# Performance work log

Hardware: AMD Instinct MI355X
Metric: run time of the kernel (lower is better)

The kernel has to match this reference:

```python
import jax, jax.numpy as jnp
import numpy as np

B, L, F, H, VOCAB = 32, 700, 4, 600, 2000  # batch, n_records(max_len), feats/record, hidden, vocab


def setup_inputs() -> dict:
    key = jax.random.key(0)
    ks = jax.random.split(key, 16)
    s = 0.02
    inp = {
        'records': jax.random.randint(ks[0], (B, L, F), 0, VOCAB, dtype=jnp.int64 if jax.config.jax_enable_x64 else jnp.int32),
        'index': jax.random.randint(ks[1], (B,), 0, L, dtype=jnp.int32),
        'emb': jax.random.normal(ks[2], (VOCAB, H), jnp.float32) * s,
        'W_relu': jax.random.normal(ks[3], (4 * H, H), jnp.float32) * s,
        'b_relu': jnp.zeros((H,), jnp.float32),
        'W_lin': jax.random.normal(ks[4], (H, H), jnp.float32) * s,
        'b_lin': jnp.zeros((H,), jnp.float32),
        'W_sig': jax.random.normal(ks[5], (2 * H, H), jnp.float32) * s,
        'b_sig': jnp.zeros((H,), jnp.float32),
        'W_ih': jax.random.normal(ks[6], (H, 4 * H), jnp.float32) * s,
        'W_hh': jax.random.normal(ks[7], (H, 4 * H), jnp.float32) * s,
        'b_ih': jnp.zeros((4 * H,), jnp.float32),
        'b_hh': jnp.zeros((4 * H,), jnp.float32),
        'W_log': jax.random.normal(ks[8], (H, L), jnp.float32) * s,
        'b_log': jnp.zeros((L,), jnp.float32),
    }
    return inp


def _select_content(records, emb, W_relu, b_relu, W_lin, b_lin, W_sig, b_sig):
    # embedding + concat of the 4 record features -> [B, L, 4H]
    embedded = emb[records]                               # [B, L, 4, H]
    emb_cat = embedded.reshape(records.shape[0], records.shape[1], -1)
    emb_relu = jax.nn.relu(emb_cat @ W_relu + b_relu)      # [B, L, H]
    emb_lin = emb_relu @ W_lin + b_lin                     # [B, L, H]
    pre_attn = jnp.einsum('bld,bmd->blm', emb_lin, emb_relu)  # [B, L, L]
    pad = (records.max(axis=2) == 0)                       # [B, L]
    mask = jnp.eye(records.shape[1], dtype=bool)[None] | pad[:, :, None] | pad[:, None, :]
    pre_attn = jnp.where(mask, -jnp.inf, pre_attn)
    attention = jax.nn.softmax(pre_attn, axis=2)
    emb_att = jnp.einsum('blm,bmd->bld', attention, emb_relu)  # [B, L, H]
    gate = jax.nn.sigmoid(jnp.concatenate([emb_relu, emb_att], axis=2) @ W_sig + b_sig)
    return gate * emb_relu                                 # selected_content [B, L, H]


def reference(records, index, emb, W_relu, b_relu, W_lin, b_lin, W_sig, b_sig,
              W_ih, W_hh, b_ih, b_hh, W_log, b_log):
    sc = _select_content(records, emb, W_relu, b_relu, W_lin, b_lin, W_sig, b_sig)
    # init_hidden
    hidden = jnp.mean(sc, axis=1)                          # [B, H]
    cell = jnp.zeros_like(hidden)
    pad_mask = (records.max(axis=2) == 0)                  # [B, L]
    # forward (one pointer step)
    b_idx = jnp.arange(records.shape[0])
    mask = pad_mask.at[b_idx, index].set(True)             # scatter_(1, index, 1)
    x = sc[b_idx, index]                                   # gather -> [B, H]
    gates = x @ W_ih + hidden @ W_hh + b_ih + b_hh         # [B, 4H]
    i, f, g, o = jnp.split(gates, 4, axis=1)               # torch LSTM gate order
    cell = jax.nn.sigmoid(f) * cell + jax.nn.sigmoid(i) * jnp.tanh(g)
    hidden = jax.nn.sigmoid(o) * jnp.tanh(cell)
    logits = hidden @ W_log + b_log                        # [B, max_len]
    masked = jnp.where(mask, -jnp.inf, logits)
    attention = jax.nn.log_softmax(masked, axis=1)         # [B, max_len]
    return attention, hidden, cell
```

## Files before the change

kernel.cpp:

```cpp
#include <hip/hip_runtime.h>
#include <math.h>

typedef unsigned short u16;
typedef _Float16 half8 __attribute__((ext_vector_type(8)));
typedef float f32x4 __attribute__((ext_vector_type(4)));

#define BB 32
#define LL 700
#define HH 600
#define VV 2000
#define H4 2400

#define O_SCAT   0L
#define O_LINH   57344000L
#define O_R1     86016000L
#define O_ATTNH  112896000L
#define O_ERT    144435200L
#define O_EMBH   171468800L
#define O_W2T    174028800L
#define O_WLT    177100800L
#define O_WST    177920000L
#define O_BL     179456000L
#define O_PAD    179458560L
#define O_GATES  179624960L
#define O_WIHT   179932160L
#define O_WLOGT  186076160L
#define O_XCAT   186977280L
#define O_HID16  187059200L
#define O_GLOG   187100160L
#define O_XMEAN  187190272L

__device__ inline u16 f2h(float x) { _Float16 h = (_Float16)x; u16 u; __builtin_memcpy(&u, &h, 2); return u; }
__device__ inline float h2f(u16 u) { _Float16 h; __builtin_memcpy(&h, &u, 2); return (float)h; }
__device__ inline float to_f(float x) { return x; }
__device__ inline float to_f(u16 x) { return h2f(x); }

__device__ __forceinline__ void gll16(const u16* g, u16* l) {
    __builtin_amdgcn_global_load_lds(
        (__attribute__((address_space(1))) void*)g,
        (__attribute__((address_space(3))) void*)l, 16, 0, 0);
}

template<int EPI>
__global__ __launch_bounds__(512, 4) void hgemm_v2(
    const u16* __restrict__ A, const u16* __restrict__ B,
    u16* __restrict__ C16, const float* __restrict__ bias,
    const u16* __restrict__ gate, int ldg,
    float* __restrict__ xmean,
    int M, int N, int Kp, int lda, int ldb, int ldc,
    long sAz, long sBz, long sCz)
{
    const int bz = blockIdx.z;
    A += sAz * bz;  B += sBz * bz;  C16 += sCz * bz;

    __shared__ __align__(16) u16 As[16384];
    __shared__ __align__(16) u16 Bs[16384];

    const int tid = threadIdx.x;

    const int nx = gridDim.x, ny = gridDim.y;
    const int bid = blockIdx.y * nx + blockIdx.x;
    const int fg  = ny >> 3;
    const int gsz = nx << 3;
    int m_i, n_i;
    if (bid < fg * gsz) {
        int g = bid / gsz, r = bid - g * gsz;
        m_i = (g << 3) + (r & 7);
        n_i = r >> 3;
    } else {
        m_i = bid / nx;
        n_i = bid - m_i * nx;
    }
    const int m0 = m_i << 7, n0 = n_i << 7;

    const int wave = tid >> 6, lane = tid & 63;
    const int fr = lane & 15, q = lane >> 4;
    const int s0 = (q ^ (fr & 7)) << 3;
    const int wm = (wave >> 2) << 6;
    const int wn = (wave & 3) << 5;

    const int srow = lane >> 3;
    const int kx   = ((lane & 7) ^ srow) << 3;
    int ra0 = m0 + (wave << 4) + srow;       if (ra0 > M - 1) ra0 = M - 1;
    int ra1 = m0 + (wave << 4) + 8 + srow;   if (ra1 > M - 1) ra1 = M - 1;
    int rb0 = n0 + (wave << 4) + srow;       if (rb0 > N - 1) rb0 = N - 1;
    int rb1 = n0 + (wave << 4) + 8 + srow;   if (rb1 > N - 1) rb1 = N - 1;
    const u16* gA0 = A + (long)ra0 * lda + kx;
    const u16* gA1 = A + (long)ra1 * lda + kx;
    const u16* gB0 = B + (long)rb0 * ldb + kx;
    const u16* gB1 = B + (long)rb1 * ldb + kx;
    u16* sAw = (u16*)As + (wave << 10);
    u16* sBw = (u16*)Bs + (wave << 10);

    f32x4 acc[4][2];
    #pragma unroll
    for (int i = 0; i < 4; ++i)
        #pragma unroll
        for (int j = 0; j < 2; ++j) acc[i][j] = (f32x4)0.f;

    const int nk = Kp >> 6;

    gll16(gA0, sAw);  gll16(gA1, sAw + 512);
    gll16(gB0, sBw);  gll16(gB1, sBw + 512);
    __syncthreads();

    for (int t = 0; t < nk; ++t) {
        const int cur = (t & 1) << 13;
        if (t + 1 < nk) {
            const int nxt = cur ^ 8192;
            const long ko = (long)(t + 1) << 6;
            gll16(gA0 + ko, sAw + nxt);  gll16(gA1 + ko, sAw + nxt + 512);
            gll16(gB0 + ko, sBw + nxt);  gll16(gB1 + ko, sBw + nxt + 512);
        }
        #pragma unroll
        for (int half = 0; half < 2; ++half) {
            const int sh = s0 ^ (half << 5);
            half8 af[4], bf[2];
            #pragma unroll
            for (int i = 0; i < 4; ++i)
                af[i] = *(const half8*)&As[cur + ((wm + (i << 4) + fr) << 6) + sh];
            #pragma unroll
            for (int j = 0; j < 2; ++j)
                bf[j] = *(const half8*)&Bs[cur + ((wn + (j << 4) + fr) << 6) + sh];
            #pragma unroll
            for (int i = 0; i < 4; ++i)
                #pragma unroll
                for (int j = 0; j < 2; ++j)
                    acc[i][j] = __builtin_amdgcn_mfma_f32_16x16x32_f16(af[i], bf[j], acc[i][j], 0, 0, 0);
        }
        __syncthreads();
    }

    const int lr = (lane >> 4) << 2;
    #pragma unroll
    for (int j = 0; j < 2; ++j) {
        int n = n0 + wn + (j << 4) + fr;
        if (n >= N) continue;
        float bv = bias ? bias[n] : 0.f;
        float ps = 0.f;
        int   cb = -1;
        #pragma unroll
        for (int i = 0; i < 4; ++i) {
            #pragma unroll
            for (int r = 0; r < 4; ++r) {
                int m = m0 + wm + (i << 4) + lr + r;
                if (m >= M) continue;
                long off = (long)m * ldc + n;
                float v = acc[i][j][r] + bv;
                if (EPI == 1) C16[off] = f2h(v);
                if (EPI == 2) {
                    float sg = 1.f / (1.f + expf(-v));
                    float scv = sg * h2f(gate[(long)m * ldg + n]);
                    C16[off] = f2h(scv);
                    int b = m / 700;
                    if (b != cb) {
                        if (cb >= 0) atomicAdd(&xmean[cb * 640 + n], ps);
                        cb = b;  ps = 0.f;
                    }
                    ps += scv;
                }
            }
        }
        if (EPI == 2 && cb >= 0) atomicAdd(&xmean[cb * 640 + n], ps);
    }
}

__global__ __launch_bounds__(256) void sgemm_k(
    const u16* __restrict__ A, const u16* __restrict__ B, float* __restrict__ C,
    int N, int Kseg, int lda, int ldb, int ldc)
{
    const int wave = threadIdx.x >> 6, lane = threadIdx.x & 63;
    const int fr = lane & 15, q8 = (lane >> 4) << 3;
    int n = blockIdx.x * 64 + wave * 16 + fr;
    int nc = (n < N) ? n : N - 1;
    const int k0 = blockIdx.y * Kseg;
    const u16* pa0 = A + (long)fr * lda + q8;
    const u16* pa1 = A + (long)(fr + 16) * lda + q8;
    const u16* pb  = B + (long)nc * ldb + q8;
    f32x4 acc0 = (f32x4)0.f, acc1 = (f32x4)0.f;
    #pragma unroll 2
    for (int k = k0; k < k0 + Kseg; k += 32) {
        half8 a0 = *(const half8*)(pa0 + k);
        half8 a1 = *(const half8*)(pa1 + k);
        half8 bv = *(const half8*)(pb + k);
        acc0 = __builtin_amdgcn_mfma_f32_16x16x32_f16(a0, bv, acc0, 0, 0, 0);
        acc1 = __builtin_amdgcn_mfma_f32_16x16x32_f16(a1, bv, acc1, 0, 0, 0);
    }
    if (n >= N) return;
    const int mr = (lane >> 4) << 2;
    #pragma unroll
    for (int r = 0; r < 4; ++r) {
        atomicAdd(&C[(long)(mr + r) * ldc + n], acc0[r]);
        atomicAdd(&C[(long)(mr + r + 16) * ldc + n], acc1[r]);
    }
}

__global__ __launch_bounds__(256) void prep_k(
    const float* __restrict__ emb, const float* __restrict__ W_relu,
    const float* __restrict__ W_lin, const float* __restrict__ W_sig,
    const float* __restrict__ W_ih, const float* __restrict__ W_hh,
    const float* __restrict__ W_log, const float* __restrict__ b_lin,
    const float* __restrict__ b_ih, const float* __restrict__ b_hh,
    const float* __restrict__ b_log,
    u16* __restrict__ embh, u16* __restrict__ w2t, u16* __restrict__ wlt,
    u16* __restrict__ wst, u16* __restrict__ wiht, u16* __restrict__ wlogt,
    float* __restrict__ bl640, float* __restrict__ gates, float* __restrict__ glog,
    float* __restrict__ xmean)
{
    __shared__ float t[32][33];
    const int z = blockIdx.z, bx = blockIdx.x, by = blockIdx.y;
    const int tid = threadIdx.x;

    if (z == 10) {
        int r = by * 32 + (tid >> 5), c = bx * 32 + (tid & 31);
        #pragma unroll
        for (int dy = 0; dy < 32; dy += 8) {
            int rr = r + dy;
            if (rr < VV && c < 640)
                embh[(long)rr * 640 + c] = (c < 600) ? f2h(emb[(long)rr * 600 + c]) : 0;
        }
        return;
    }
    if (z == 11) {
        long idx = ((long)bx * 75 + by) * 256 + tid;
        const long NG = 640 + (long)BB * H4;
        const long NL = NG + (long)BB * 704;
        const long NX = NL + (long)BB * 640;
        if (idx < 640) {
            bl640[idx] = (idx < 600) ? b_lin[idx] : 0.f;
        } else if (idx < NG) {
            long i = idx - 640;
            int n = (int)(i % H4);
            gates[i] = b_ih[n] + b_hh[n];
        } else if (idx < NL) {
            long i = idx - NG;
            int l = (int)(i % 704);
            glog[i] = (l < 700) ? b_log[l] : 0.f;
        } else if (idx < NX) {
            xmean[idx - NL] = 0.f;
        }
        return;
    }

    const float* s; u16* d;
    int R, C, lds_, ldo, Rpad, Cpad;
    if (z < 4)      { s = W_relu + 360000L * z; d = w2t + 384000L * z;
                      R = 600; C = 600; lds_ = 600; ldo = 640;  Rpad = 640; Cpad = 600; }
    else if (z == 4){ s = W_lin;           d = wlt;
                      R = 600; C = 600; lds_ = 600; ldo = 640;  Rpad = 640; Cpad = 640; }
    else if (z == 5){ s = W_sig;           d = wst;
                      R = 600; C = 600; lds_ = 600; ldo = 1280; Rpad = 640; Cpad = 600; }
    else if (z == 6){ s = W_sig + 360000;  d = wst + 640;
                      R = 600; C = 600; lds_ = 600; ldo = 1280; Rpad = 640; Cpad = 600; }
    else if (z == 7){ s = W_ih;            d = wiht;
                      R = 600; C = H4;  lds_ = H4;  ldo = 1280; Rpad = 640; Cpad = H4; }
    else if (z == 8){ s = W_hh;            d = wiht + 640;
                      R = 600; C = H4;  lds_ = H4;  ldo = 1280; Rpad = 640; Cpad = H4; }
    else            { s = W_log;           d = wlogt;
                      R = 600; C = 700; lds_ = 700; ldo = 640;  Rpad = 640; Cpad = 704; }

    int r0 = bx * 32, c0 = by * 32;
    if (r0 >= Rpad || c0 >= Cpad) return;
    int tx = tid & 31, ty = tid >> 5;
    #pragma unroll
    for (int dy = 0; dy < 32; dy += 8) {
        int r = r0 + ty + dy, c = c0 + tx;
        t[ty + dy][tx] = (r < R && c < C) ? s[(long)r * lds_ + c] : 0.f;
    }
    __syncthreads();
    #pragma unroll
    for (int dy = 0; dy < 32; dy += 8) {
        int c = c0 + ty + dy, r = r0 + tx;
        if (r < Rpad && c < Cpad) d[(long)c * ldo + r] = f2h(t[tx][ty + dy]);
    }
}

template<typename T>
__global__ __launch_bounds__(256) void transpz_k(
    const T* __restrict__ s, u16* __restrict__ d,
    int R, int C, int lds_, int ldo, int Rpad, int Cpad, long zs_s, long zs_d)
{
    __shared__ float t[32][33];
    s += zs_s * blockIdx.z;  d += zs_d * blockIdx.z;
    int r0 = blockIdx.x * 32, c0 = blockIdx.y * 32;
    int tx = threadIdx.x & 31, ty = threadIdx.x >> 5;
    #pragma unroll
    for (int dy = 0; dy < 32; dy += 8) {
        int r = r0 + ty + dy, c = c0 + tx;
        t[ty + dy][tx] = (r < R && c < C) ? to_f(s[(long)r * lds_ + c]) : 0.f;
    }
    __syncthreads();
    #pragma unroll
    for (int dy = 0; dy < 32; dy += 8) {
        int c = c0 + ty + dy, r = r0 + tx;
        if (r < Rpad && c < Cpad) d[(long)c * ldo + r] = f2h(t[tx][ty + dy]);
    }
}

__global__ __launch_bounds__(320) void gather_relu_k(
    const int* __restrict__ rec, const u16* __restrict__ Ph,
    const float* __restrict__ b_relu, u16* __restrict__ scat, float* __restrict__ pad)
{
    int row = blockIdx.x;
    int t = threadIdx.x;
    int r0 = rec[row * 4 + 0], r1 = rec[row * 4 + 1];
    int r2 = rec[row * 4 + 2], r3 = rec[row * 4 + 3];
    u16* srow = scat + (long)row * 1280;
    if (t < 300) {
        int h = t << 1;
        uint a0 = *(const uint*)&Ph[(long)r0 * H4 + h];
        uint a1 = *(const uint*)&Ph[(long)r1 * H4 + 600 + h];
        uint a2 = *(const uint*)&Ph[(long)r2 * H4 + 1200 + h];
        uint a3 = *(const uint*)&Ph[(long)r3 * H4 + 1800 + h];
        float lo = b_relu[h]     + h2f((u16)a0) + h2f((u16)a1) + h2f((u16)a2) + h2f((u16)a3);
        float hi = b_relu[h + 1] + h2f((u16)(a0 >> 16)) + h2f((u16)(a1 >> 16))
                                 + h2f((u16)(a2 >> 16)) + h2f((u16)(a3 >> 16));
        uint o = (uint)f2h(fmaxf(lo, 0.f)) | ((uint)f2h(fmaxf(hi, 0.f)) << 16);
        *(uint*)&srow[h] = o;
    } else {
        int i = t - 300;
        *(uint*)&srow[600 + (i << 1)]  = 0;
        *(uint*)&srow[1240 + (i << 1)] = 0;
    }
    if (t == 0) {
        int mx = max(max(r0, r1), max(r2, r3));
        pad[row] = (mx == 0) ? 1.f : 0.f;
    }
}

__global__ __launch_bounds__(256) void softmax_w(u16* __restrict__ attnh,
                                                 const float* __restrict__ pad)
{
    const int wave = threadIdx.x >> 6, lane = threadIdx.x & 63;
    const int l = blockIdx.x * 4 + wave, b = blockIdx.y;
    u16* row = attnh + (long)b * (LL * 704) + (long)l * 704;
    const float* pb = pad + b * LL;
    const bool rowpad = pb[l] != 0.f;

    float v[12];
    float mx = -INFINITY;
    #pragma unroll
    for (int i = 0; i < 6; ++i) {
        int e0 = (lane + (i << 6)) << 1;
        float x0 = -INFINITY, x1 = -INFINITY;
        if (e0 < 704) {
            uint u = *(const uint*)&row[e0];
            if (e0 < LL && !(rowpad || e0 == l || pb[e0] != 0.f)) x0 = h2f((u16)u);
            int e1 = e0 + 1;
            if (e1 < LL && !(rowpad || e1 == l || pb[e1] != 0.f)) x1 = h2f((u16)(u >> 16));
        }
        v[2 * i] = x0;  v[2 * i + 1] = x1;
        mx = fmaxf(mx, fmaxf(x0, x1));
    }
    #pragma unroll
    for (int m = 32; m > 0; m >>= 1) mx = fmaxf(mx, __shfl_xor(mx, m));
    mx = fmaxf(mx, -1e30f);

    float sum = 0.f;
    #pragma unroll
    for (int i = 0; i < 12; ++i) { v[i] = expf(v[i] - mx); sum += v[i]; }
    #pragma unroll
    for (int m = 32; m > 0; m >>= 1) sum += __shfl_xor(sum, m);
    float inv = (sum > 0.f) ? 1.f / sum : 0.f;

    #pragma unroll
    for (int i = 0; i < 6; ++i) {
        int e0 = (lane + (i << 6)) << 1;
        if (e0 < 704) {
            uint u = (uint)f2h(v[2 * i] * inv) | ((uint)f2h(v[2 * i + 1] * inv) << 16);
            *(uint*)&row[e0] = u;
        }
    }
}

__global__ __launch_bounds__(256) void xcat_k(const u16* __restrict__ sc,
                                              const int* __restrict__ index,
                                              const float* __restrict__ xmean,
                                              u16* __restrict__ xcat)
{
    int b = blockIdx.y;
    if (blockIdx.x == 3) {
        const u16* src = sc + ((long)b * LL + index[b]) * HH;
        u16* dst = xcat + b * 1280;
        for (int j = threadIdx.x; j < 1280; j += 256) {
            if (j < 600) dst[j] = src[j];
            else if (j < 640) dst[j] = 0;
            else if (j >= 1240) dst[j] = 0;
        }
        return;
    }
    int h = blockIdx.x * 256 + threadIdx.x;
    if (h >= HH) return;
    xcat[b * 1280 + 640 + h] = f2h(xmean[b * 640 + h] * (1.f / 700.f));
}

__global__ void lstm_act_k(const float* __restrict__ gates,
                           float* __restrict__ out_hid, float* __restrict__ out_cell,
                           u16* __restrict__ hid16)
{
    int h = blockIdx.x * 256 + threadIdx.x;
    int b = blockIdx.y;
    if (h >= 640) return;
    if (h >= HH) { hid16[b * 640 + h] = 0; return; }
    const float* g = gates + b * H4;
    float gi = g[h], gg = g[1200 + h], go = g[1800 + h];
    float c = (1.f / (1.f + expf(-gi))) * tanhf(gg);
    float hd = (1.f / (1.f + expf(-go))) * tanhf(c);
    out_hid[b * HH + h] = hd;
    out_cell[b * HH + h] = c;
    hid16[b * 640 + h] = f2h(hd);
}

__global__ __launch_bounds__(256) void logsoftmax_k(const float* __restrict__ glog,
                                                    const float* __restrict__ pad,
                                                    const int* __restrict__ index,
                                                    float* __restrict__ out)
{
    int b = blockIdx.x;
    int t = threadIdx.x;
    int idx = index[b];
    __shared__ float red[256];
    float v[3];
    float mx = -INFINITY;
    #pragma unroll
    for (int ii = 0; ii < 3; ++ii) {
        int l = ii * 256 + t;
        float x = -INFINITY;
        if (l < LL && !(pad[b * LL + l] != 0.f || l == idx)) x = glog[b * 704 + l];
        v[ii] = x;
        mx = fmaxf(mx, x);
    }
    red[t] = mx; __syncthreads();
    for (int s = 128; s > 0; s >>= 1) {
        if (t < s) red[t] = fmaxf(red[t], red[t + s]);
        __syncthreads();
    }
    mx = red[0]; __syncthreads();
    float sum = 0.f;
    #pragma unroll
    for (int ii = 0; ii < 3; ++ii) {
        int l = ii * 256 + t;
        if (l < LL) sum += expf(v[ii] - mx);
    }
    red[t] = sum; __syncthreads();
    for (int s = 128; s > 0; s >>= 1) {
        if (t < s) red[t] += red[t + s];
        __syncthreads();
    }
    float lse = mx + logf(red[0]);
    #pragma unroll
    for (int ii = 0; ii < 3; ++ii) {
        int l = ii * 256 + t;
        if (l < LL) out[b * LL + l] = fmaxf(v[ii] - lse, -1e30f);
    }
}

extern "C" void kernel_launch(void* const* d_in, const int* in_sizes, int n_in,
                              void* d_out, int out_size, void* d_ws, size_t ws_size,
                              hipStream_t stream)
{
    const int*   records = (const int*)d_in[0];
    const int*   index   = (const int*)d_in[1];
    const float* emb     = (const float*)d_in[2];
    const float* W_relu  = (const float*)d_in[3];
    const float* b_relu  = (const float*)d_in[4];
    const float* W_lin   = (const float*)d_in[5];
    const float* b_lin   = (const float*)d_in[6];
    const float* W_sig   = (const float*)d_in[7];
    const float* b_sig   = (const float*)d_in[8];
    const float* W_ih    = (const float*)d_in[9];
    const float* W_hh    = (const float*)d_in[10];
    const float* b_ih    = (const float*)d_in[11];
    const float* b_hh    = (const float*)d_in[12];
    const float* W_log   = (const float*)d_in[13];
    const float* b_log   = (const float*)d_in[14];

    char* ws = (char*)d_ws;
    u16*   scat   = (u16*)(ws + O_SCAT);
    u16*   linh   = (u16*)(ws + O_LINH);
    u16*   Ph     = (u16*)(ws + O_R1);
    u16*   sc16   = (u16*)(ws + O_R1);
    u16*   attnh  = (u16*)(ws + O_ATTNH);
    u16*   erT    = (u16*)(ws + O_ERT);
    u16*   embh   = (u16*)(ws + O_EMBH);
    u16*   w2t    = (u16*)(ws + O_W2T);
    u16*   wlt    = (u16*)(ws + O_WLT);
    u16*   wst    = (u16*)(ws + O_WST);
    float* bl640  = (float*)(ws + O_BL);
    float* pad    = (float*)(ws + O_PAD);
    float* gates  = (float*)(ws + O_GATES);
    u16*   wiht   = (u16*)(ws + O_WIHT);
    u16*   wlogt  = (u16*)(ws + O_WLOGT);
    u16*   xcat   = (u16*)(ws + O_XCAT);
    u16*   hid16  = (u16*)(ws + O_HID16);
    float* glog   = (float*)(ws + O_GLOG);
    float* xmean  = (float*)(ws + O_XMEAN);

    float* out      = (float*)d_out;
    float* out_attn = out;
    float* out_hid  = out + BB * LL;
    float* out_cell = out + BB * LL + BB * HH;

    prep_k<<<dim3(20, 75, 12), 256, 0, stream>>>(
        emb, W_relu, W_lin, W_sig, W_ih, W_hh, W_log, b_lin, b_ih, b_hh, b_log,
        embh, w2t, wlt, wst, wiht, wlogt, bl640, gates, glog, xmean);

    hgemm_v2<1><<<dim3(19, 16, 1), 512, 0, stream>>>(
        embh, w2t, Ph, nullptr, nullptr, 0, nullptr,
        VV, H4, 640, 640, 640, H4, 0L, 0L, 0L);

    gather_relu_k<<<dim3(BB * LL), 320, 0, stream>>>(records, Ph, b_relu, scat, pad);

    hgemm_v2<1><<<dim3(5, 175, 1), 512, 0, stream>>>(
        scat, wlt, linh, bl640, nullptr, 0, nullptr,
        BB * LL, 640, 640, 1280, 640, 640, 0L, 0L, 0L);

    hgemm_v2<1><<<dim3(6, 6, BB), 512, 0, stream>>>(
        linh, scat, attnh, nullptr, nullptr, 0, nullptr,
        LL, LL, 640, 640, 1280, 704, (long)LL * 640, (long)LL * 1280, (long)LL * 704);

    softmax_w<<<dim3(175, BB), 256, 0, stream>>>(attnh, pad);

    transpz_k<u16><<<dim3(22, 19, BB), 256, 0, stream>>>(
        scat, erT, 700, 600, 1280, 704, 704, 600, (long)700 * 1280, (long)600 * 704);

    hgemm_v2<1><<<dim3(5, 6, BB), 512, 0, stream>>>(
        attnh, erT, scat + 640, nullptr, nullptr, 0, nullptr,
        LL, HH, 704, 704, 704, 1280, (long)LL * 704, (long)HH * 704, (long)LL * 1280);

    hgemm_v2<2><<<dim3(5, 175, 1), 512, 0, stream>>>(
        scat, wst, sc16, b_sig, scat, 1280, xmean,
        BB * LL, HH, 1280, 1280, 1280, 600, 0L, 0L, 0L);

    xcat_k<<<dim3(4, BB), 256, 0, stream>>>(sc16, index, xmean, xcat);
    sgemm_k<<<dim3(38, 5), 256, 0, stream>>>(
        xcat, wiht, gates, H4, 256, 1280, 1280, H4);
    lstm_act_k<<<dim3(3, BB), 256, 0, stream>>>(gates, out_hid, out_cell, hid16);
    sgemm_k<<<dim3(11, 5), 256, 0, stream>>>(
        hid16, wlogt, glog, LL, 128, 640, 640, 704);
    logsoftmax_k<<<dim3(BB), 256, 0, stream>>>(glog, pad, index, out_attn);
}
```

Before: 426.9 us.

## Load weight B-operand directly from global in weight GEMMs; fast xmean epilogue

Adds a BDIR template mode where the B (weight) fragments are read straight from global memory into registers instead of being staged through LDS. This halves LDS use and drops the B copy traffic for the three weight-side GEMMs, where the small weight matrix is likely to stay in cache. The EPI==2 epilogue gains an interior fast path: when a wave's 64 rows fall inside one batch, it reduces the column partial sums with shuffles and issues one atomic per column instead of per-lane atomics with per-row division. The cost is that B reads now come from global or cache with the latency exposed inside the MFMA loop.

```diff
diff --git a/kernel.cpp b/kernel.cpp
--- a/kernel.cpp
+++ b/kernel.cpp
@@ -41,7 +41,7 @@
         (__attribute__((address_space(3))) void*)l, 16, 0, 0);
 }
 
-template<int EPI>
+template<int EPI, int BDIR>
 __global__ __launch_bounds__(512, 4) void hgemm_v2(
     const u16* __restrict__ A, const u16* __restrict__ B,
     u16* __restrict__ C16, const float* __restrict__ bias,
@@ -54,7 +54,7 @@
     A += sAz * bz;  B += sBz * bz;  C16 += sCz * bz;
 
     __shared__ __align__(16) u16 As[16384];
-    __shared__ __align__(16) u16 Bs[16384];
+    __shared__ __align__(16) u16 Bs[BDIR ? 16 : 16384];
 
     const int tid = threadIdx.x;
 
@@ -83,14 +83,25 @@
     const int kx   = ((lane & 7) ^ srow) << 3;
     int ra0 = m0 + (wave << 4) + srow;       if (ra0 > M - 1) ra0 = M - 1;
     int ra1 = m0 + (wave << 4) + 8 + srow;   if (ra1 > M - 1) ra1 = M - 1;
-    int rb0 = n0 + (wave << 4) + srow;       if (rb0 > N - 1) rb0 = N - 1;
-    int rb1 = n0 + (wave << 4) + 8 + srow;   if (rb1 > N - 1) rb1 = N - 1;
     const u16* gA0 = A + (long)ra0 * lda + kx;
     const u16* gA1 = A + (long)ra1 * lda + kx;
-    const u16* gB0 = B + (long)rb0 * ldb + kx;
-    const u16* gB1 = B + (long)rb1 * ldb + kx;
     u16* sAw = (u16*)As + (wave << 10);
-    u16* sBw = (u16*)Bs + (wave << 10);
+
+    const u16 *gB0 = nullptr, *gB1 = nullptr;
+    u16* sBw = nullptr;
+    const u16 *pB0 = nullptr, *pB1 = nullptr;
+    if (!BDIR) {
+        int rb0 = n0 + (wave << 4) + srow;       if (rb0 > N - 1) rb0 = N - 1;
+        int rb1 = n0 + (wave << 4) + 8 + srow;   if (rb1 > N - 1) rb1 = N - 1;
+        gB0 = B + (long)rb0 * ldb + kx;
+        gB1 = B + (long)rb1 * ldb + kx;
+        sBw = (u16*)Bs + (wave << 10);
+    } else {
+        int nb0 = n0 + wn + fr;        if (nb0 > N - 1) nb0 = N - 1;
+        int nb1 = n0 + wn + 16 + fr;   if (nb1 > N - 1) nb1 = N - 1;
+        pB0 = B + (long)nb0 * ldb + (q << 3);
+        pB1 = B + (long)nb1 * ldb + (q << 3);
+    }
 
     f32x4 acc[4][2];
     #pragma unroll
@@ -101,7 +112,7 @@
     const int nk = Kp >> 6;
 
     gll16(gA0, sAw);  gll16(gA1, sAw + 512);
-    gll16(gB0, sBw);  gll16(gB1, sBw + 512);
+    if (!BDIR) { gll16(gB0, sBw);  gll16(gB1, sBw + 512); }
     __syncthreads();
 
     for (int t = 0; t < nk; ++t) {
@@ -110,7 +121,7 @@
             const int nxt = cur ^ 8192;
             const long ko = (long)(t + 1) << 6;
             gll16(gA0 + ko, sAw + nxt);  gll16(gA1 + ko, sAw + nxt + 512);
-            gll16(gB0 + ko, sBw + nxt);  gll16(gB1 + ko, sBw + nxt + 512);
+            if (!BDIR) { gll16(gB0 + ko, sBw + nxt);  gll16(gB1 + ko, sBw + nxt + 512); }
         }
         #pragma unroll
         for (int half = 0; half < 2; ++half) {
@@ -119,9 +130,15 @@
             #pragma unroll
             for (int i = 0; i < 4; ++i)
                 af[i] = *(const half8*)&As[cur + ((wm + (i << 4) + fr) << 6) + sh];
-            #pragma unroll
-            for (int j = 0; j < 2; ++j)
-                bf[j] = *(const half8*)&Bs[cur + ((wn + (j << 4) + fr) << 6) + sh];
+            if (BDIR) {
+                const long ko = ((long)t << 6) + (half << 5);
+                bf[0] = *(const half8*)(pB0 + ko);
+                bf[1] = *(const half8*)(pB1 + ko);
+            } else {
+                #pragma unroll
+                for (int j = 0; j < 2; ++j)
+                    bf[j] = *(const half8*)&Bs[cur + ((wn + (j << 4) + fr) << 6) + sh];
+            }
             #pragma unroll
             for (int i = 0; i < 4; ++i)
                 #pragma unroll
@@ -132,36 +149,66 @@
     }
 
     const int lr = (lane >> 4) << 2;
+
+    int  bb0 = 0, bound = 0;
+    bool interior = false;
+    if (EPI == 2) {
+        const int mlo = m0 + wm, mhi = m0 + wm + 63;
+        bb0   = mlo / 700;
+        bound = (bb0 + 1) * 700;
+        interior = (mhi < bound) && (mhi < M);
+    }
+
     #pragma unroll
     for (int j = 0; j < 2; ++j) {
         int n = n0 + wn + (j << 4) + fr;
         if (n >= N) continue;
         float bv = bias ? bias[n] : 0.f;
-        float ps = 0.f;
-        int   cb = -1;
-        #pragma unroll
-        for (int i = 0; i < 4; ++i) {
+
+        if (EPI == 2 && interior) {
+            float ps = 0.f;
             #pragma unroll
-            for (int r = 0; r < 4; ++r) {
-                int m = m0 + wm + (i << 4) + lr + r;
-                if (m >= M) continue;
-                long off = (long)m * ldc + n;
-                float v = acc[i][j][r] + bv;
-                if (EPI == 1) C16[off] = f2h(v);
-                if (EPI == 2) {
+            for (int i = 0; i < 4; ++i) {
+                #pragma unroll
+                for (int r = 0; r < 4; ++r) {
+                    int m = m0 + wm + (i << 4) + lr + r;
+                    float v = acc[i][j][r] + bv;
                     float sg = 1.f / (1.f + expf(-v));
                     float scv = sg * h2f(gate[(long)m * ldg + n]);
-                    C16[off] = f2h(scv);
-                    int b = m / 700;
-                    if (b != cb) {
-                        if (cb >= 0) atomicAdd(&xmean[cb * 640 + n], ps);
-                        cb = b;  ps = 0.f;
-                    }
+                    C16[(long)m * ldc + n] = f2h(scv);
                     ps += scv;
                 }
             }
-        }
-        if (EPI == 2 && cb >= 0) atomicAdd(&xmean[cb * 640 + n], ps);
+            ps += __shfl_xor(ps, 16);
+            ps += __shfl_xor(ps, 32);
+            if (q == 0) atomicAdd(&xmean[bb0 * 640 + n], ps);
+        } else {
+            float ps = 0.f;
+            int   cb = -1;
+            #pragma unroll
+            for (int i = 0; i < 4; ++i) {
+                #pragma unroll
+                for (int r = 0; r < 4; ++r) {
+                    int m = m0 + wm + (i << 4) + lr + r;
+                    if (m >= M) continue;
+                    long off = (long)m * ldc + n;
+                    float v = acc[i][j][r] + bv;
+                    if (EPI == 1) C16[off] = f2h(v);
+                    if (EPI == 2) {
+                        float sg = 1.f / (1.f + expf(-v));
+                        float scv = sg * h2f(gate[(long)m * ldg + n]);
+                        C16[off] = f2h(scv);
+                        int b = (m < bound) ? bb0 : bb0 + 1;
+                        if (b != cb) {
+                            if (cb >= 0) atomicAdd(&xmean[cb * 640 + n], ps);
+                            cb = b;  ps = 0.f;
+                        }
+                        ps += scv;
+                    }
+                }
+            }
+            if (EPI == 2 && cb >= 0) atomicAdd(&xmean[cb * 640 + n], ps);
+        }
     }
 }
 
@@ -505,17 +552,17 @@
         emb, W_relu, W_lin, W_sig, W_ih, W_hh, W_log, b_lin, b_ih, b_hh, b_log,
         embh, w2t, wlt, wst, wiht, wlogt, bl640, gates, glog, xmean);
 
-    hgemm_v2<1><<<dim3(19, 16, 1), 512, 0, stream>>>(
+    hgemm_v2<1, 1><<<dim3(19, 16, 1), 512, 0, stream>>>(
         embh, w2t, Ph, nullptr, nullptr, 0, nullptr,
         VV, H4, 640, 640, 640, H4, 0L, 0L, 0L);
 
     gather_relu_k<<<dim3(BB * LL), 320, 0, stream>>>(records, Ph, b_relu, scat, pad);
 
-    hgemm_v2<1><<<dim3(5, 175, 1), 512, 0, stream>>>(
+    hgemm_v2<1, 1><<<dim3(5, 175, 1), 512, 0, stream>>>(
         scat, wlt, linh, bl640, nullptr, 0, nullptr,
         BB * LL, 640, 640, 1280, 640, 640, 0L, 0L, 0L);
 
-    hgemm_v2<1><<<dim3(6, 6, BB), 512, 0, stream>>>(
+    hgemm_v2<1, 0><<<dim3(6, 6, BB), 512, 0, stream>>>(
         linh, scat, attnh, nullptr, nullptr, 0, nullptr,
         LL, LL, 640, 640, 1280, 704, (long)LL * 640, (long)LL * 1280, (long)LL * 704);
 
@@ -524,11 +571,11 @@
     transpz_k<u16><<<dim3(22, 19, BB), 256, 0, stream>>>(
         scat, erT, 700, 600, 1280, 704, 704, 600, (long)700 * 1280, (long)600 * 704);
 
-    hgemm_v2<1><<<dim3(5, 6, BB), 512, 0, stream>>>(
+    hgemm_v2<1, 0><<<dim3(5, 6, BB), 512, 0, stream>>>(
         attnh, erT, scat + 640, nullptr, nullptr, 0, nullptr,
         LL, HH, 704, 704, 704, 1280, (long)LL * 704, (long)HH * 704, (long)LL * 1280);
 
-    hgemm_v2<2><<<dim3(5, 175, 1), 512, 0, stream>>>(
+    hgemm_v2<2, 1><<<dim3(5, 175, 1), 512, 0, stream>>>(
         scat, wst, sc16, b_sig, scat, 1280, xmean,
         BB * LL, HH, 1280, 1280, 1280, 600, 0L, 0L, 0L);
 
```

Result: slower. 496.6 us (+16.3%).
